# Optimization experiments

Measured on AMD Instinct MI355X. Metric: run time of the kernel, lower is better.

The kernel has to match this reference:

```python
import jax, jax.numpy as jnp
import numpy as np

DIM = 256
NUM_HEADS = 8
KS = 3
DILATIONS = (1, 2, 3, 4)
HEAD_DIM = DIM // NUM_HEADS
SCALE = HEAD_DIM ** -0.5
HIDDEN = 4 * DIM


def setup_inputs() -> dict:
    key = jax.random.key(0)
    ks = jax.random.split(key, 8)
    B, H, W = 4, 64, 64

    def w(k, shape):
        return jax.random.normal(k, shape, jnp.float32) * 0.02

    return {
        "x": jax.random.normal(ks[0], (2, B, DIM, H, W), jnp.float32),
        "norm1_w": jnp.ones((2, DIM), jnp.float32),
        "norm1_b": jnp.zeros((2, DIM), jnp.float32),
        "q_w": w(ks[1], (2, DIM, DIM)),
        "k_w": w(ks[2], (2, DIM, DIM)),
        "v_w": w(ks[3], (2, DIM, DIM)),
        "proj_w": w(ks[4], (2, DIM, DIM)),
        "proj_b": jnp.zeros((2, DIM), jnp.float32),
        "norm2_w": jnp.ones((2, DIM), jnp.float32),
        "norm2_b": jnp.zeros((2, DIM), jnp.float32),
        "fc1_w": w(ks[5], (2, HIDDEN, DIM)),
        "fc1_b": jnp.zeros((2, HIDDEN), jnp.float32),
        "fc2_w": w(ks[6], (2, DIM, HIDDEN)),
        "fc2_b": jnp.zeros((2, DIM), jnp.float32),
    }


def _layer_norm(x, w, b, eps=1e-5):
    mu = jnp.mean(x, -1, keepdims=True)
    var = jnp.mean((x - mu) ** 2, -1, keepdims=True)
    return (x - mu) * jax.lax.rsqrt(var + eps) * w + b


def _unfold(x, ks, dil):
    # x: (B, d, H, W) -> (B, d, ks*ks, H, W); zero-padded dilated local patches
    # matches nn.Unfold(ks, dilation=dil, padding=dil*(ks-1)//2): channel-major,
    # kernel positions row-major inner.
    B, d, H, W = x.shape
    p = dil * (ks - 1) // 2
    xp = jnp.pad(x, ((0, 0), (0, 0), (p, p), (p, p)))
    pats = [xp[:, :, i * dil:i * dil + H, j * dil:j * dil + W]
            for i in range(ks) for j in range(ks)]
    return jnp.stack(pats, axis=2)


def _dilate_attn(q, k, v, dil):
    # q,k,v: (B, d, H, W) with d = DIM // num_dilation
    B, d, H, W = q.shape
    h = d // HEAD_DIM
    N = H * W
    kk = KS * KS
    qh = q.reshape(B, h, HEAD_DIM, N)                        # b h c n
    kp = _unfold(k, KS, dil).reshape(B, h, HEAD_DIM, kk, N)  # b h c k n
    attn = jnp.einsum('bhcn,bhckn->bhnk', qh, kp) * SCALE    # b h n kk
    attn = jax.nn.softmax(attn, axis=-1)
    vp = _unfold(v, KS, dil).reshape(B, h, HEAD_DIM, kk, N)
    out = jnp.einsum('bhnk,bhckn->bhnc', attn, vp)           # b h n c
    return out.transpose(0, 2, 1, 3).reshape(B, H, W, d)     # B H W d


def _mda(x1, x2, x3, qw, kw, vw, pw, pb):
    # MultiDilatelocalAttention; x*: (B, H, W, C)
    nd = len(DILATIONS)
    cd = DIM // nd
    q = jnp.einsum('bhwc,oc->bohw', x1, qw)  # 1x1 conv, no bias
    k = jnp.einsum('bhwc,oc->bohw', x2, kw)
    v = jnp.einsum('bhwc,oc->bohw', x3, vw)
    outs = [_dilate_attn(q[:, i * cd:(i + 1) * cd], k[:, i * cd:(i + 1) * cd],
                         v[:, i * cd:(i + 1) * cd], DILATIONS[i])
            for i in range(nd)]
    x = jnp.concatenate(outs, axis=-1)  # (B, H, W, C)
    return x @ pw.T + pb


def _block(x1, x2, x3, p, bi):
    # DilateBlock; inputs BCHW
    x1, x2, x3 = (t.transpose(0, 2, 3, 1) for t in (x1, x2, x3))
    n1 = lambda t: _layer_norm(t, p['norm1_w'][bi], p['norm1_b'][bi])
    x = x1 + _mda(n1(x1), n1(x2), n1(x3), p['q_w'][bi], p['k_w'][bi],
                  p['v_w'][bi], p['proj_w'][bi], p['proj_b'][bi])
    h = _layer_norm(x, p['norm2_w'][bi], p['norm2_b'][bi])
    h = jax.nn.gelu(h @ p['fc1_w'][bi].T + p['fc1_b'][bi], approximate=False)
    x = x + h @ p['fc2_w'][bi].T + p['fc2_b'][bi]
    return x.transpose(0, 3, 1, 2)


def reference(x, norm1_w, norm1_b, q_w, k_w, v_w, proj_w, proj_b,
              norm2_w, norm2_b, fc1_w, fc1_b, fc2_w, fc2_b):
    p = dict(norm1_w=norm1_w, norm1_b=norm1_b, q_w=q_w, k_w=k_w, v_w=v_w,
             proj_w=proj_w, proj_b=proj_b, norm2_w=norm2_w, norm2_b=norm2_b,
             fc1_w=fc1_w, fc1_b=fc1_b, fc2_w=fc2_w, fc2_b=fc2_b)
    vi, ir = x[0], x[1]
    vi_ir_div = _block(vi - ir, ir, ir, p, 0)
    ir_vi_div = _block(ir - vi, vi, vi, p, 1)
    return (vi_ir_div, ir_vi_div)
```

## Files before the change

kernel.cpp:

```cpp
#include <hip/hip_runtime.h>
#include <hip/hip_bf16.h>

typedef __attribute__((ext_vector_type(8))) short bf16x8;
typedef __attribute__((ext_vector_type(4))) float f32x4;

#define HWSZ 4096
#define NPIX 16384

__device__ inline float b2f(short s) {
  return __uint_as_float(((unsigned)(unsigned short)s) << 16);
}
__device__ inline short f2b(float f) {
  __hip_bfloat16 h = __float2bfloat16(f);
  return *(short*)&h;
}
__device__ inline void gl16(const short* g, short* l) {
  __builtin_amdgcn_global_load_lds(
      (const __attribute__((address_space(1))) unsigned int*)g,
      (__attribute__((address_space(3))) unsigned int*)l, 16, 0, 0);
}
__device__ inline float gelu_f(float x) {
  float ax = fabsf(x) * 0.70710678118654752f;
  float t = 1.f / (1.f + 0.3275911f * ax);
  float y = t * (0.254829592f + t * (-0.284496736f + t * (1.421413741f +
            t * (-1.453152027f + t * 1.061405429f))));
  float erfv = 1.f - y * __expf(-ax * ax);
  erfv = copysignf(erfv, x);
  return 0.5f * x * (1.f + erfv);
}

__global__ __launch_bounds__(256) void convert_k(
    const float* __restrict__ qw, const float* __restrict__ kw,
    const float* __restrict__ vw, const float* __restrict__ pw,
    const float* __restrict__ f1, const float* __restrict__ f2,
    __hip_bfloat16* __restrict__ out)
{
  int idx = blockIdx.x * 256 + threadIdx.x;
  if (idx >= 2 * 786432) return;
  int bi = idx / 786432;
  int r  = idx - bi * 786432;
  float v;
  if      (r <  65536) v = qw[bi*65536 + r];
  else if (r < 131072) v = kw[bi*65536 + r - 65536];
  else if (r < 196608) v = vw[bi*65536 + r - 131072];
  else if (r < 262144) v = pw[bi*65536 + r - 196608];
  else if (r < 524288) v = f1[bi*262144 + r - 262144];
  else                 v = f2[bi*262144 + r - 524288];
  out[idx] = __float2bfloat16(v);
}

__global__ __launch_bounds__(256) void prep2_k(
    const float* __restrict__ x,
    const float* __restrict__ nw, const float* __restrict__ nb,
    __hip_bfloat16* __restrict__ ln1a,
    __hip_bfloat16* __restrict__ ln1b,
    __hip_bfloat16* __restrict__ diff,
    float av, float ai, float bv, float bb)
{
  __shared__ float t1[16][257], t2[16][257];
  __shared__ float red[4][16][16];
  __shared__ float mu1[16], rs1[16], mu2[16], rs2[16];
  int t = threadIdx.x;
  int pix0 = blockIdx.x * 16;
  int b = pix0 >> 12, hw0 = pix0 & 4095;
  const float* vi = x + (size_t)b * 256 * HWSZ;
  const float* ir = x + (size_t)(4 + b) * 256 * HWSZ;

  for (int it = 0; it < 16; ++it) {
    int idx = it * 256 + t;
    int p = idx & 15, c = idx >> 4;
    size_t off = (size_t)c * HWSZ + hw0 + p;
    float a = vi[off], bb2 = ir[off];
    t1[p][c] = av * a + ai * bb2;
    t2[p][c] = bv * a + bb * bb2;
  }
  __syncthreads();
  {
    int p = t & 15, q = t >> 4;
    float s1 = 0, ss1 = 0, s2 = 0, ss2 = 0;
    for (int i = 0; i < 16; ++i) {
      float v = t1[p][q*16 + i]; s1 += v; ss1 += v*v;
      float u = t2[p][q*16 + i]; s2 += u; ss2 += u*u;
    }
    red[0][p][q] = s1; red[1][p][q] = ss1; red[2][p][q] = s2; red[3][p][q] = ss2;
  }
  __syncthreads();
  if (t < 32) {
    int p = t & 15, which = t >> 4;
    float s = 0, ss = 0;
    for (int q = 0; q < 16; ++q) { s += red[which*2][p][q]; ss += red[which*2+1][p][q]; }
    float mu = s * (1.f/256.f);
    float var = ss * (1.f/256.f) - mu*mu;
    float rs = rsqrtf(var + 1e-5f);
    if (which == 0) { mu1[p] = mu; rs1[p] = rs; }
    else            { mu2[p] = mu; rs2[p] = rs; }
  }
  __syncthreads();
  for (int it = 0; it < 16; ++it) {
    float v1 = t1[it][t], v2 = t2[it][t];
    size_t o = (size_t)(pix0 + it) * 256 + t;
    ln1a[o] = __float2bfloat16((v1 - mu1[it]) * rs1[it] * nw[t] + nb[t]);
    ln1b[o] = __float2bfloat16((v2 - mu2[it]) * rs2[it] * nw[t] + nb[t]);
    diff[o] = __float2bfloat16(v1);
  }
}

template<int EPI>
__global__ __launch_bounds__(256) void gemm6_k(
    const short* __restrict__ A, const short* __restrict__ W,
    void* __restrict__ outp, const float* __restrict__ bias,
    const short* __restrict__ res, int K, int ldc)
{
  __shared__ __align__(16) short As[2][64 * 32];
  __shared__ __align__(16) short Bs[2][64 * 32];
  int tid = threadIdx.x;
  int l = tid & 63, wv = tid >> 6;
  int wm = wv >> 1, wn = wv & 1;
  int m0 = blockIdx.x * 64;
  int n0 = blockIdx.y * 64;
  int lr = l & 15, lq = l >> 4;

  int srow = tid >> 2;
  int sch = (tid & 3) ^ ((srow >> 1) & 3);
  const short* gA = A + (size_t)(m0 + srow) * K + sch * 8;
  const short* gB = W + (size_t)(n0 + srow) * K + sch * 8;

  f32x4 acc[2][2];
  #pragma unroll
  for (int mi = 0; mi < 2; ++mi)
    #pragma unroll
    for (int ni = 0; ni < 2; ++ni) acc[mi][ni] = (f32x4){0.f, 0.f, 0.f, 0.f};

  gl16(gA, &As[0][0] + tid * 8);
  gl16(gB, &Bs[0][0] + tid * 8);
  __syncthreads();

  int cur = 0;
  int rowa0 = wm * 32 + lr;
  int rowb0 = wn * 32 + lr;
  for (int k0 = 0; k0 < K; k0 += 32) {
    int kn = k0 + 32;
    if (kn < K) {
      gl16(gA + kn, &As[cur ^ 1][0] + tid * 8);
      gl16(gB + kn, &Bs[cur ^ 1][0] + tid * 8);
    }
    bf16x8 af[2], bfr[2];
    #pragma unroll
    for (int mi = 0; mi < 2; ++mi) {
      int row = rowa0 + mi * 16;
      int kc = lq ^ ((row >> 1) & 3);
      af[mi] = *(const bf16x8*)(&As[cur][0] + row * 32 + kc * 8);
    }
    #pragma unroll
    for (int ni = 0; ni < 2; ++ni) {
      int row = rowb0 + ni * 16;
      int kc = lq ^ ((row >> 1) & 3);
      bfr[ni] = *(const bf16x8*)(&Bs[cur][0] + row * 32 + kc * 8);
    }
    #pragma unroll
    for (int mi = 0; mi < 2; ++mi)
      #pragma unroll
      for (int ni = 0; ni < 2; ++ni)
        acc[mi][ni] = __builtin_amdgcn_mfma_f32_16x16x32_bf16(af[mi], bfr[ni], acc[mi][ni], 0, 0, 0);
    __syncthreads();
    cur ^= 1;
  }

  #pragma unroll
  for (int mi = 0; mi < 2; ++mi)
  #pragma unroll
  for (int ni = 0; ni < 2; ++ni) {
    #pragma unroll
    for (int r = 0; r < 4; ++r) {
      int row = m0 + wm * 32 + mi * 16 + lq * 4 + r;
      int col = n0 + wn * 32 + ni * 16 + lr;
      float v = acc[mi][ni][r];
      if (EPI == 0) {
        ((short*)outp)[(size_t)row * ldc + col] = f2b(v);
      } else if (EPI == 1) {
        v += bias[col] + b2f(res[(size_t)row * 256 + col]);
        ((short*)outp)[(size_t)row * 256 + col] = f2b(v);
      } else if (EPI == 2) {
        v = gelu_f(v + bias[col]);
        ((short*)outp)[(size_t)row * ldc + col] = f2b(v);
      } else {
        v += bias[col] + b2f(res[(size_t)row * 256 + col]);
        int b = row >> 12, hw = row & 4095;
        ((float*)outp)[(size_t)(b * 256 + col) * HWSZ + hw] = v;
      }
    }
  }
}

__global__ __launch_bounds__(256) void attn2_k(
    const __hip_bfloat16* __restrict__ Q,
    const __hip_bfloat16* __restrict__ KV,
    __hip_bfloat16* __restrict__ out)
{
  int gid = blockIdx.x * 256 + threadIdx.x;
  int pix = gid >> 3, head = gid & 7;
  int dil = (head >> 1) + 1;
  int y = (pix >> 6) & 63, xc = pix & 63;
  int base = pix & ~4095;
  const short* q8 = (const short*)Q + (size_t)pix * 256 + head * 32;
  float qf[32];
  #pragma unroll
  for (int j = 0; j < 4; ++j) {
    bf16x8 v = *(const bf16x8*)(q8 + j * 8);
    #pragma unroll
    for (int e = 0; e < 8; ++e) qf[j*8 + e] = b2f(v[e]);
  }
  float lg[9];
  int npx[9];
  #pragma unroll
  for (int t = 0; t < 9; ++t) {
    int ny = y + (t / 3 - 1) * dil;
    int nx = xc + (t % 3 - 1) * dil;
    bool ok = ((unsigned)ny < 64u) && ((unsigned)nx < 64u);
    npx[t] = ok ? (base | (ny * 64 + nx)) : -1;
    float d = 0.f;
    if (ok) {
      const short* k8 = (const short*)KV + (size_t)npx[t] * 512 + head * 32;
      #pragma unroll
      for (int j = 0; j < 4; ++j) {
        bf16x8 v = *(const bf16x8*)(k8 + j * 8);
        #pragma unroll
        for (int e = 0; e < 8; ++e) d += qf[j*8 + e] * b2f(v[e]);
      }
    }
    lg[t] = d * 0.17677669529663687f;
  }
  float m = lg[0];
  #pragma unroll
  for (int t = 1; t < 9; ++t) m = fmaxf(m, lg[t]);
  float w[9], den = 0.f;
  #pragma unroll
  for (int t = 0; t < 9; ++t) { w[t] = expf(lg[t] - m); den += w[t]; }
  float inv = 1.f / den;
  float acc[32];
  #pragma unroll
  for (int j = 0; j < 32; ++j) acc[j] = 0.f;
  #pragma unroll
  for (int t = 0; t < 9; ++t) {
    if (npx[t] >= 0) {
      const short* v8 = (const short*)KV + (size_t)npx[t] * 512 + 256 + head * 32;
      float wt = w[t];
      #pragma unroll
      for (int j = 0; j < 4; ++j) {
        bf16x8 v = *(const bf16x8*)(v8 + j * 8);
        #pragma unroll
        for (int e = 0; e < 8; ++e) acc[j*8 + e] += wt * b2f(v[e]);
      }
    }
  }
  short* op = (short*)out + (size_t)pix * 256 + head * 32;
  #pragma unroll
  for (int j = 0; j < 4; ++j) {
    bf16x8 o;
    #pragma unroll
    for (int e = 0; e < 8; ++e) o[e] = f2b(acc[j*8 + e] * inv);
    *(bf16x8*)(op + j * 8) = o;
  }
}

__global__ __launch_bounds__(256) void ln2b_k(
    const __hip_bfloat16* __restrict__ xm, const float* __restrict__ w2,
    const float* __restrict__ b2, __hip_bfloat16* __restrict__ h)
{
  int pix = blockIdx.x * 4 + (threadIdx.x >> 6);
  int l = threadIdx.x & 63;
  const short* p = (const short*)xm + (size_t)pix * 256 + l * 4;
  short4 sv = *(const short4*)p;
  float vv[4] = {b2f(sv.x), b2f(sv.y), b2f(sv.z), b2f(sv.w)};
  float s = vv[0] + vv[1] + vv[2] + vv[3];
  float ss = vv[0]*vv[0] + vv[1]*vv[1] + vv[2]*vv[2] + vv[3]*vv[3];
  #pragma unroll
  for (int off = 32; off; off >>= 1) { s += __shfl_xor(s, off); ss += __shfl_xor(ss, off); }
  float mu = s * (1.f/256.f);
  float rstd = rsqrtf(ss * (1.f/256.f) - mu*mu + 1e-5f);
  #pragma unroll
  for (int j = 0; j < 4; ++j) {
    int c = l * 4 + j;
    h[(size_t)pix * 256 + c] = __float2bfloat16((vv[j] - mu) * rstd * w2[c] + b2[c]);
  }
}

extern "C" void kernel_launch(void* const* d_in, const int* in_sizes, int n_in,
                              void* d_out, int out_size, void* d_ws, size_t ws_size,
                              hipStream_t stream)
{
  const float* x   = (const float*)d_in[0];
  const float* n1w = (const float*)d_in[1];
  const float* n1b = (const float*)d_in[2];
  const float* qw  = (const float*)d_in[3];
  const float* kw  = (const float*)d_in[4];
  const float* vw  = (const float*)d_in[5];
  const float* pw  = (const float*)d_in[6];
  const float* pb  = (const float*)d_in[7];
  const float* n2w = (const float*)d_in[8];
  const float* n2b = (const float*)d_in[9];
  const float* f1w = (const float*)d_in[10];
  const float* f1b = (const float*)d_in[11];
  const float* f2w = (const float*)d_in[12];
  const float* f2b = (const float*)d_in[13];
  float* outp = (float*)d_out;
  char* ws = (char*)d_ws;

  const size_t MB = 1024 * 1024;
  __hip_bfloat16* wbf   = (__hip_bfloat16*)(ws);
  __hip_bfloat16* ln1a  = (__hip_bfloat16*)(ws + 3*MB);
  __hip_bfloat16* attnb = (__hip_bfloat16*)(ws + 3*MB);
  __hip_bfloat16* h     = (__hip_bfloat16*)(ws + 3*MB);
  __hip_bfloat16* ln1b  = (__hip_bfloat16*)(ws + 11*MB);
  __hip_bfloat16* diff  = (__hip_bfloat16*)(ws + 19*MB);
  __hip_bfloat16* qbuf  = (__hip_bfloat16*)(ws + 27*MB);
  __hip_bfloat16* kv    = (__hip_bfloat16*)(ws + 35*MB);
  __hip_bfloat16* xmid  = (__hip_bfloat16*)(ws + 35*MB);
  __hip_bfloat16* hb    = (__hip_bfloat16*)(ws + 43*MB);

  convert_k<<<6144, 256, 0, stream>>>(qw, kw, vw, pw, f1w, f2w, wbf);

  for (int bi = 0; bi < 2; ++bi) {
    const short* wq  = (const short*)(wbf + (size_t)bi * 786432);
    const short* wkv = wq + 65536;
    const short* wp  = wq + 196608;
    const short* w1  = wq + 262144;
    const short* w2  = wq + 524288;
    float av = (bi == 0) ? 1.f : -1.f, ai = (bi == 0) ? -1.f : 1.f;
    float bv = (bi == 0) ? 0.f : 1.f,  bb = (bi == 0) ? 1.f : 0.f;

    prep2_k<<<1024, 256, 0, stream>>>(x, n1w + bi*256, n1b + bi*256, ln1a, ln1b, diff, av, ai, bv, bb);

    gemm6_k<0><<<dim3(256, 4), 256, 0, stream>>>(
        (const short*)ln1a, wq, qbuf, nullptr, nullptr, 256, 256);
    gemm6_k<0><<<dim3(256, 8), 256, 0, stream>>>(
        (const short*)ln1b, wkv, kv, nullptr, nullptr, 256, 512);

    attn2_k<<<512, 256, 0, stream>>>(qbuf, kv, attnb);

    gemm6_k<1><<<dim3(256, 4), 256, 0, stream>>>(
        (const short*)attnb, wp, xmid, pb + bi*256, (const short*)diff, 256, 256);
    ln2b_k<<<4096, 256, 0, stream>>>(xmid, n2w + bi*256, n2b + bi*256, hb);

    gemm6_k<2><<<dim3(256, 16), 256, 0, stream>>>(
        (const short*)hb, w1, h, f1b + bi*1024, nullptr, 256, 1024);
    gemm6_k<3><<<dim3(256, 4), 256, 0, stream>>>(
        (const short*)h, w2, outp + (size_t)bi * 4194304, f2b + bi*256, (const short*)xmid, 1024, 256);
  }
}
```

Measured before the change: 250.9 us.

## Merge Q and KV GEMMs, widen FC1 tile, vectorize transposed output stores

Pulls the GEMM body into a templated device function parameterized by N-tile width. The Q and KV projections now run as one launch that picks its input, weight and output from blockIdx.y, which removes a launch and gives a single larger grid. FC1 uses a 128-wide N tile so each block reuses its A tile across twice as many columns, at the cost of more registers and LDS per block. The final NCHW fp32 store writes float4 along the pixel dimension instead of scalar strided stores.

```diff
diff --git a/kernel.cpp b/kernel.cpp
--- a/kernel.cpp
+++ b/kernel.cpp
@@ -105,46 +105,48 @@
   }
 }
 
-template<int EPI>
-__global__ __launch_bounds__(256) void gemm6_k(
+template<int EPI, int BN>
+__device__ __forceinline__ void gemm_core(
     const short* __restrict__ A, const short* __restrict__ W,
     void* __restrict__ outp, const float* __restrict__ bias,
-    const short* __restrict__ res, int K, int ldc)
-{
+    const short* __restrict__ res, int K, int ldc, int m0, int n0)
+{
+  constexpr int NI = (BN == 128) ? 4 : 2;
   __shared__ __align__(16) short As[2][64 * 32];
-  __shared__ __align__(16) short Bs[2][64 * 32];
+  __shared__ __align__(16) short Bs[2][BN * 32];
   int tid = threadIdx.x;
   int l = tid & 63, wv = tid >> 6;
   int wm = wv >> 1, wn = wv & 1;
-  int m0 = blockIdx.x * 64;
-  int n0 = blockIdx.y * 64;
   int lr = l & 15, lq = l >> 4;
 
   int srow = tid >> 2;
   int sch = (tid & 3) ^ ((srow >> 1) & 3);
   const short* gA = A + (size_t)(m0 + srow) * K + sch * 8;
   const short* gB = W + (size_t)(n0 + srow) * K + sch * 8;
-
-  f32x4 acc[2][2];
+  const short* gB1 = (BN == 128) ? (W + (size_t)(n0 + srow + 64) * K + sch * 8) : nullptr;
+
+  f32x4 acc[2][NI];
   #pragma unroll
   for (int mi = 0; mi < 2; ++mi)
     #pragma unroll
-    for (int ni = 0; ni < 2; ++ni) acc[mi][ni] = (f32x4){0.f, 0.f, 0.f, 0.f};
+    for (int ni = 0; ni < NI; ++ni) acc[mi][ni] = (f32x4){0.f, 0.f, 0.f, 0.f};
 
   gl16(gA, &As[0][0] + tid * 8);
   gl16(gB, &Bs[0][0] + tid * 8);
+  if constexpr (BN == 128) gl16(gB1, &Bs[0][0] + 2048 + tid * 8);
   __syncthreads();
 
   int cur = 0;
   int rowa0 = wm * 32 + lr;
-  int rowb0 = wn * 32 + lr;
+  int rowb0 = wn * (BN / 2) + lr;
   for (int k0 = 0; k0 < K; k0 += 32) {
     int kn = k0 + 32;
     if (kn < K) {
       gl16(gA + kn, &As[cur ^ 1][0] + tid * 8);
       gl16(gB + kn, &Bs[cur ^ 1][0] + tid * 8);
-    }
-    bf16x8 af[2], bfr[2];
+      if constexpr (BN == 128) gl16(gB1 + kn, &Bs[cur ^ 1][0] + 2048 + tid * 8);
+    }
+    bf16x8 af[2], bfr[NI];
     #pragma unroll
     for (int mi = 0; mi < 2; ++mi) {
       int row = rowa0 + mi * 16;
@@ -152,7 +154,7 @@
       af[mi] = *(const bf16x8*)(&As[cur][0] + row * 32 + kc * 8);
     }
     #pragma unroll
-    for (int ni = 0; ni < 2; ++ni) {
+    for (int ni = 0; ni < NI; ++ni) {
       int row = rowb0 + ni * 16;
       int kc = lq ^ ((row >> 1) & 3);
       bfr[ni] = *(const bf16x8*)(&Bs[cur][0] + row * 32 + kc * 8);
@@ -160,7 +162,7 @@
     #pragma unroll
     for (int mi = 0; mi < 2; ++mi)
       #pragma unroll
-      for (int ni = 0; ni < 2; ++ni)
+      for (int ni = 0; ni < NI; ++ni)
         acc[mi][ni] = __builtin_amdgcn_mfma_f32_16x16x32_bf16(af[mi], bfr[ni], acc[mi][ni], 0, 0, 0);
     __syncthreads();
     cur ^= 1;
@@ -169,27 +171,57 @@
   #pragma unroll
   for (int mi = 0; mi < 2; ++mi)
   #pragma unroll
-  for (int ni = 0; ni < 2; ++ni) {
-    #pragma unroll
-    for (int r = 0; r < 4; ++r) {
-      int row = m0 + wm * 32 + mi * 16 + lq * 4 + r;
-      int col = n0 + wn * 32 + ni * 16 + lr;
-      float v = acc[mi][ni][r];
-      if (EPI == 0) {
-        ((short*)outp)[(size_t)row * ldc + col] = f2b(v);
-      } else if (EPI == 1) {
-        v += bias[col] + b2f(res[(size_t)row * 256 + col]);
-        ((short*)outp)[(size_t)row * 256 + col] = f2b(v);
-      } else if (EPI == 2) {
-        v = gelu_f(v + bias[col]);
-        ((short*)outp)[(size_t)row * ldc + col] = f2b(v);
-      } else {
-        v += bias[col] + b2f(res[(size_t)row * 256 + col]);
-        int b = row >> 12, hw = row & 4095;
-        ((float*)outp)[(size_t)(b * 256 + col) * HWSZ + hw] = v;
+  for (int ni = 0; ni < NI; ++ni) {
+    int row0 = m0 + wm * 32 + mi * 16 + lq * 4;
+    int col = n0 + wn * (BN / 2) + ni * 16 + lr;
+    if (EPI == 3) {
+      float bc = bias[col];
+      float4 o;
+      #pragma unroll
+      for (int r = 0; r < 4; ++r)
+        ((float*)&o)[r] = acc[mi][ni][r] + bc + b2f(res[(size_t)(row0 + r) * 256 + col]);
+      int b = row0 >> 12, hw = row0 & 4095;
+      *(float4*)((float*)outp + (size_t)(b * 256 + col) * HWSZ + hw) = o;
+    } else {
+      #pragma unroll
+      for (int r = 0; r < 4; ++r) {
+        int row = row0 + r;
+        float v = acc[mi][ni][r];
+        if (EPI == 0) {
+          ((short*)outp)[(size_t)row * ldc + col] = f2b(v);
+        } else if (EPI == 1) {
+          v += bias[col] + b2f(res[(size_t)row * 256 + col]);
+          ((short*)outp)[(size_t)row * 256 + col] = f2b(v);
+        } else {
+          v = gelu_f(v + bias[col]);
+          ((short*)outp)[(size_t)row * ldc + col] = f2b(v);
+        }
       }
     }
   }
+}
+
+template<int EPI, int BN>
+__global__ __launch_bounds__(256) void gemm6_k(
+    const short* __restrict__ A, const short* __restrict__ W,
+    void* __restrict__ outp, const float* __restrict__ bias,
+    const short* __restrict__ res, int K, int ldc)
+{
+  gemm_core<EPI, BN>(A, W, outp, bias, res, K, ldc, blockIdx.x * 64, blockIdx.y * BN);
+}
+
+__global__ __launch_bounds__(256) void qkv_k(
+    const short* __restrict__ ln1a, const short* __restrict__ ln1b,
+    const short* __restrict__ wq, const short* __restrict__ wkv,
+    short* __restrict__ qbuf, short* __restrict__ kv)
+{
+  bool isQ = blockIdx.y < 4;
+  const short* A = isQ ? ln1a : ln1b;
+  const short* W = isQ ? wq : wkv;
+  void* outp = isQ ? (void*)qbuf : (void*)kv;
+  int ldc = isQ ? 256 : 512;
+  int n0 = (isQ ? blockIdx.y : (blockIdx.y - 4)) * 64;
+  gemm_core<0, 64>(A, W, outp, nullptr, nullptr, 256, ldc, blockIdx.x * 64, n0);
 }
 
 __global__ __launch_bounds__(256) void attn2_k(
@@ -331,20 +363,18 @@
 
     prep2_k<<<1024, 256, 0, stream>>>(x, n1w + bi*256, n1b + bi*256, ln1a, ln1b, diff, av, ai, bv, bb);
 
-    gemm6_k<0><<<dim3(256, 4), 256, 0, stream>>>(
-        (const short*)ln1a, wq, qbuf, nullptr, nullptr, 256, 256);
-    gemm6_k<0><<<dim3(256, 8), 256, 0, stream>>>(
-        (const short*)ln1b, wkv, kv, nullptr, nullptr, 256, 512);
+    qkv_k<<<dim3(256, 12), 256, 0, stream>>>(
+        (const short*)ln1a, (const short*)ln1b, wq, wkv, (short*)qbuf, (short*)kv);
 
     attn2_k<<<512, 256, 0, stream>>>(qbuf, kv, attnb);
 
-    gemm6_k<1><<<dim3(256, 4), 256, 0, stream>>>(
+    gemm6_k<1, 64><<<dim3(256, 4), 256, 0, stream>>>(
         (const short*)attnb, wp, xmid, pb + bi*256, (const short*)diff, 256, 256);
     ln2b_k<<<4096, 256, 0, stream>>>(xmid, n2w + bi*256, n2b + bi*256, hb);
 
-    gemm6_k<2><<<dim3(256, 16), 256, 0, stream>>>(
+    gemm6_k<2, 128><<<dim3(256, 8), 256, 0, stream>>>(
         (const short*)hb, w1, h, f1b + bi*1024, nullptr, 256, 1024);
-    gemm6_k<3><<<dim3(256, 4), 256, 0, stream>>>(
+    gemm6_k<3, 64><<<dim3(256, 4), 256, 0, stream>>>(
         (const short*)h, w2, outp + (size_t)bi * 4194304, f2b + bi*256, (const short*)xmid, 1024, 256);
   }
 }
```

New measurement: 233.8 us. 1.07x faster.
